# Kernel optimization log

Hardware: AMD Instinct MI355X
Metric: run time of the kernel (lower is better)

## Reference

```python
import jax, jax.numpy as jnp
import numpy as np

E, D, H, T = 8, 2048, 5632, 32768  # experts, dim, hidden_dim, total routed tokens


def setup_inputs() -> dict:
    key = jax.random.key(0)
    k_x, k1, k2, k3 = jax.random.split(key, 4)
    x = jax.random.normal(k_x, (T, D), dtype=jnp.float32)
    # trunc_normal init stds per init_weights (approx: plain normal, same scale)
    std = (2.0 / (D * 24)) ** 0.5
    w1 = jax.random.normal(k1, (E, H, D), dtype=jnp.float32) * std
    w2 = jax.random.normal(k2, (E, D, H), dtype=jnp.float32) * std
    w3 = jax.random.normal(k3, (E, H, D), dtype=jnp.float32) * std
    # tokens are pre-sorted by expert; even split 4096 tokens/expert (sums to T)
    num_tokens_per_expert = jnp.full((E,), T // E, dtype=jnp.int32)
    return {"x": x, "w1": w1, "w2": w2, "w3": w3,
            "num_tokens_per_expert": num_tokens_per_expert}


def _grouped_experts(x, w1, w2, w3, counts):
    # Faithful to _run_experts_grouped_mm: grouped GEMMs computed in bf16,
    # SwiGLU activation, cast back to x dtype.
    xb = x.astype(jnp.bfloat16)
    w1b = jnp.transpose(w1.astype(jnp.bfloat16), (0, 2, 1))  # [E, D, H]
    w3b = jnp.transpose(w3.astype(jnp.bfloat16), (0, 2, 1))  # [E, D, H]
    w2b = jnp.transpose(w2.astype(jnp.bfloat16), (0, 2, 1))  # [E, H, D]
    h1 = jax.lax.ragged_dot(xb, w1b, counts)   # [T, H]
    h3 = jax.lax.ragged_dot(xb, w3b, counts)   # [T, H]
    h = jax.nn.silu(h1) * h3                   # fused SwiGLU gate
    out = jax.lax.ragged_dot(h, w2b, counts)   # [T, D]
    return out.astype(x.dtype)


def reference(x, w1, w2, w3, num_tokens_per_expert):
    return _grouped_experts(x, w1, w2, w3, num_tokens_per_expert)
```

## Files before the change

kernel.cpp:

```cpp
#include <hip/hip_runtime.h>
#include <hip/hip_bf16.h>
#include <stdint.h>

#define TT 32768
#define DD 2048
#define HH 5632
#define NE 8

typedef __bf16 bf16;
typedef __bf16 bf16x8 __attribute__((ext_vector_type(8)));
typedef float  f32x4  __attribute__((ext_vector_type(4)));

__device__ __forceinline__ void gl16(const void* g, void* l) {
    __builtin_amdgcn_global_load_lds(
        (const __attribute__((address_space(1))) void*)g,
        (__attribute__((address_space(3))) void*)l, 16, 0, 0);
}
#define VMW(n) asm volatile("s_waitcnt vmcnt(" #n ")" ::: "memory")
#define BARRIER() __builtin_amdgcn_s_barrier()

__device__ __forceinline__ int swz(int off) { return off ^ (((off >> 7) & 3) << 4); }

__device__ __forceinline__ int expert_of(const int* counts, int row0) {
    int base = 0;
    for (int i = 0; i < NE; ++i) { int c = counts[i]; if (row0 < base + c) return i; base += c; }
    return NE - 1;
}

__global__ __launch_bounds__(256)
void k_cvt(const float* __restrict__ in, bf16* __restrict__ out, long n) {
    long i = ((long)blockIdx.x * 256 + threadIdx.x) * 8;
    const long stride = (long)gridDim.x * 256 * 8;
    for (; i < n; i += stride) {
        const float4* p = (const float4*)(in + i);
        float4 a = p[0], b = p[1];
        union { bf16 v[8]; uint4 u; } r;
        r.v[0] = (bf16)a.x; r.v[1] = (bf16)a.y; r.v[2] = (bf16)a.z; r.v[3] = (bf16)a.w;
        r.v[4] = (bf16)b.x; r.v[5] = (bf16)b.y; r.v[6] = (bf16)b.z; r.v[7] = (bf16)b.w;
        *(uint4*)(out + i) = r.u;
    }
}

__global__ __launch_bounds__(512, 2)
void k_moe1(const bf16* __restrict__ xb, const bf16* __restrict__ w1b,
            const bf16* __restrict__ w3b, const int* __restrict__ counts,
            bf16* __restrict__ h) {
    extern __shared__ __align__(16) char sm[];
    const int tid = threadIdx.x;
    const int nwg = gridDim.x;
    int wg = blockIdx.x;
    wg = (wg & 7) * (nwg >> 3) + (wg >> 3);
    const int NTN = HH / 128;
    const int mt = wg / NTN, nt = wg - mt * NTN;
    const int row0 = mt * 256, col0 = nt * 128;
    const int e = expert_of(counts, row0);

    const char *sa0, *sa1, *sa2, *sa3;
    {
        int off0 = tid * 16, off1 = 8192 + tid * 16;
        int s0 = swz(off0), s1 = swz(off1);
        sa0 = (const char*)xb + (((size_t)(row0 + (s0 >> 6)) * DD) << 1) + (s0 & 63);
        sa1 = (const char*)xb + (((size_t)(row0 + (s1 >> 6)) * DD) << 1) + (s1 & 63);
        const char* w1p = (const char*)(w1b + (size_t)e * HH * DD);
        const char* w3p = (const char*)(w3b + (size_t)e * HH * DD);
        sa2 = w1p + (((size_t)(col0 + (s0 >> 6)) * DD) << 1) + (s0 & 63);
        sa3 = w3p + (((size_t)(col0 + (s0 >> 6)) * DD) << 1) + (s0 & 63);
    }
    const int dst0 = tid * 16;

    auto stage = [&](int kt) {
        char* db = sm + ((kt & 3) << 15);
        const size_t ko = (size_t)kt << 6;
        gl16(sa0 + ko, db + dst0);
        gl16(sa1 + ko, db + 8192 + dst0);
        gl16(sa2 + ko, db + 16384 + dst0);
        gl16(sa3 + ko, db + 24576 + dst0);
    };

    const int lane = tid & 63, wv = tid >> 6;
    const int wrow = wv >> 2, wcol = wv & 3;
    const int lrow = lane & 15, kb = (lane >> 4) << 4;

    int aoff[8], boff[2];
#pragma unroll
    for (int mi = 0; mi < 8; ++mi) aoff[mi] = swz((wrow * 128 + mi * 16 + lrow) * 64 + kb);
#pragma unroll
    for (int ni = 0; ni < 2; ++ni) boff[ni] = swz((wcol * 32 + ni * 16 + lrow) * 64 + kb);

    f32x4 acc1[8][2] = {};
    f32x4 acc3[8][2] = {};

    const int NT = DD / 32;
    stage(0); stage(1); stage(2);
    for (int t = 0; t < NT; ++t) {
        BARRIER();
        if (t + 3 < NT) stage(t + 3);
        const int nf = NT - 1 - t;
        if (nf >= 3) VMW(12); else if (nf == 2) VMW(8); else if (nf == 1) VMW(4); else VMW(0);
        BARRIER();
        const char* db = sm + ((t & 3) << 15);
        bf16x8 af[8], b1[2], b3[2];
#pragma unroll
        for (int mi = 0; mi < 8; ++mi) af[mi] = *(const bf16x8*)(db + aoff[mi]);
#pragma unroll
        for (int ni = 0; ni < 2; ++ni) {
            b1[ni] = *(const bf16x8*)(db + 16384 + boff[ni]);
            b3[ni] = *(const bf16x8*)(db + 24576 + boff[ni]);
        }
        __builtin_amdgcn_s_setprio(1);
#pragma unroll
        for (int mi = 0; mi < 8; ++mi)
#pragma unroll
            for (int ni = 0; ni < 2; ++ni) {
                acc1[mi][ni] = __builtin_amdgcn_mfma_f32_16x16x32_bf16(af[mi], b1[ni], acc1[mi][ni], 0, 0, 0);
                acc3[mi][ni] = __builtin_amdgcn_mfma_f32_16x16x32_bf16(af[mi], b3[ni], acc3[mi][ni], 0, 0, 0);
            }
        __builtin_amdgcn_s_setprio(0);
    }

#pragma unroll
    for (int mi = 0; mi < 8; ++mi)
#pragma unroll
        for (int ni = 0; ni < 2; ++ni)
#pragma unroll
            for (int j = 0; j < 4; ++j) {
                int row = row0 + wrow * 128 + mi * 16 + ((lane >> 4) << 2) + j;
                int col = col0 + wcol * 32 + ni * 16 + lrow;
                float f1 = (float)(bf16)acc1[mi][ni][j];
                float f3 = (float)(bf16)acc3[mi][ni][j];
                float s = f1 / (1.0f + __expf(-f1));
                h[(size_t)row * HH + col] = (bf16)(s * f3);
            }
}

__global__ __launch_bounds__(512, 2)
void k_g2(const bf16* __restrict__ hb, const bf16* __restrict__ w2b,
          const int* __restrict__ counts, float* __restrict__ out) {
    extern __shared__ __align__(16) char sm[];
    const int tid = threadIdx.x;
    const int nwg = gridDim.x;
    int wg = blockIdx.x;
    wg = (wg & 7) * (nwg >> 3) + (wg >> 3);
    const int NTN = DD / 256;
    const int mt = wg / NTN, nt = wg - mt * NTN;
    const int row0 = mt * 256, col0 = nt * 256;
    const int e = expert_of(counts, row0);

    const char *sa0, *sa1, *sa2, *sa3;
    {
        int off0 = tid * 16, off1 = 8192 + tid * 16;
        int s0 = swz(off0), s1 = swz(off1);
        sa0 = (const char*)hb + (((size_t)(row0 + (s0 >> 6)) * HH) << 1) + (s0 & 63);
        sa1 = (const char*)hb + (((size_t)(row0 + (s1 >> 6)) * HH) << 1) + (s1 & 63);
        const char* wp = (const char*)(w2b + (size_t)e * DD * HH);
        sa2 = wp + (((size_t)(col0 + (s0 >> 6)) * HH) << 1) + (s0 & 63);
        sa3 = wp + (((size_t)(col0 + (s1 >> 6)) * HH) << 1) + (s1 & 63);
    }
    const int dst0 = tid * 16;
    auto stage = [&](int kt) {
        char* db = sm + ((kt & 3) << 15);
        const size_t ko = (size_t)kt << 6;
        gl16(sa0 + ko, db + dst0);
        gl16(sa1 + ko, db + 8192 + dst0);
        gl16(sa2 + ko, db + 16384 + dst0);
        gl16(sa3 + ko, db + 24576 + dst0);
    };

    const int lane = tid & 63, wv = tid >> 6;
    const int wrow = wv >> 2, wcol = wv & 3;
    const int lrow = lane & 15, kb = (lane >> 4) << 4;

    int aoff[8], boff[4];
#pragma unroll
    for (int mi = 0; mi < 8; ++mi) aoff[mi] = swz((wrow * 128 + mi * 16 + lrow) * 64 + kb);
#pragma unroll
    for (int ni = 0; ni < 4; ++ni) boff[ni] = swz((wcol * 64 + ni * 16 + lrow) * 64 + kb);

    f32x4 acc[8][4] = {};
    const int NT = HH / 32;
    stage(0); stage(1); stage(2);
    for (int t = 0; t < NT; ++t) {
        BARRIER();
        if (t + 3 < NT) stage(t + 3);
        const int nf = NT - 1 - t;
        if (nf >= 3) VMW(12); else if (nf == 2) VMW(8); else if (nf == 1) VMW(4); else VMW(0);
        BARRIER();
        const char* db = sm + ((t & 3) << 15);
        bf16x8 af[8], bf[4];
#pragma unroll
        for (int mi = 0; mi < 8; ++mi) af[mi] = *(const bf16x8*)(db + aoff[mi]);
#pragma unroll
        for (int ni = 0; ni < 4; ++ni) bf[ni] = *(const bf16x8*)(db + 16384 + boff[ni]);
        __builtin_amdgcn_s_setprio(1);
#pragma unroll
        for (int mi = 0; mi < 8; ++mi)
#pragma unroll
            for (int ni = 0; ni < 4; ++ni)
                acc[mi][ni] = __builtin_amdgcn_mfma_f32_16x16x32_bf16(af[mi], bf[ni], acc[mi][ni], 0, 0, 0);
        __builtin_amdgcn_s_setprio(0);
    }
#pragma unroll
    for (int mi = 0; mi < 8; ++mi)
#pragma unroll
        for (int ni = 0; ni < 4; ++ni)
#pragma unroll
            for (int j = 0; j < 4; ++j) {
                int row = row0 + wrow * 128 + mi * 16 + ((lane >> 4) << 2) + j;
                int col = col0 + wcol * 64 + ni * 16 + lrow;
                out[(size_t)row * DD + col] = (float)(bf16)acc[mi][ni][j];
            }
}

__device__ __forceinline__ void stage_b_f32(const float* __restrict__ W,
                                            int n0, int k0, int ldk,
                                            int srow, int scol,
                                            bf16* __restrict__ lB) {
#pragma unroll
    for (int r = 0; r < 4; ++r) {
        int row = r * 32 + srow;
        const float4* s = (const float4*)(W + (size_t)(n0 + row) * ldk + k0 + scol);
        float4 a = s[0], b = s[1];
        union { bf16 v[8]; uint4 u; } t;
        t.v[0] = (bf16)a.x; t.v[1] = (bf16)a.y; t.v[2] = (bf16)a.z; t.v[3] = (bf16)a.w;
        t.v[4] = (bf16)b.x; t.v[5] = (bf16)b.y; t.v[6] = (bf16)b.z; t.v[7] = (bf16)b.w;
        *(uint4*)&lB[row * 64 + scol] = t.u;
    }
}

__global__ __launch_bounds__(256, 2)
void k_gemm1_fb(const bf16* __restrict__ xb, const float* __restrict__ w1,
                const float* __restrict__ w3, const int* __restrict__ counts,
                bf16* __restrict__ hbuf) {
    __shared__ bf16 lA[128 * 64];
    __shared__ bf16 lB1[128 * 64];
    __shared__ bf16 lB3[128 * 64];
    const int tid = threadIdx.x;
    const int col0 = blockIdx.x * 128, row0 = blockIdx.y * 128;
    const int e = expert_of(counts, row0);
    const float* W1 = w1 + (size_t)e * HH * DD;
    const float* W3 = w3 + (size_t)e * HH * DD;
    const int lane = tid & 63, wv = tid >> 6;
    const int wr = wv >> 1, wc = wv & 1;
    const int lrow = lane & 15, lk8 = (lane >> 4) * 8;
    const int srow = tid >> 3, scol = (tid & 7) * 8;
    f32x4 acc1[4][4] = {}; f32x4 acc3[4][4] = {};
    for (int k0 = 0; k0 < DD; k0 += 64) {
#pragma unroll
        for (int r = 0; r < 4; ++r) {
            int row = r * 32 + srow;
            gl16(xb + (size_t)(row0 + row) * DD + k0 + scol, &lA[row * 64 + scol]);
        }
        stage_b_f32(W1, col0, k0, DD, srow, scol, lB1);
        stage_b_f32(W3, col0, k0, DD, srow, scol, lB3);
        __syncthreads();
#pragma unroll
        for (int kk = 0; kk < 64; kk += 32) {
            bf16x8 av[4], b1v[4], b3v[4];
#pragma unroll
            for (int mi = 0; mi < 4; ++mi) av[mi] = *(const bf16x8*)&lA[(wr * 64 + mi * 16 + lrow) * 64 + kk + lk8];
#pragma unroll
            for (int ni = 0; ni < 4; ++ni) {
                b1v[ni] = *(const bf16x8*)&lB1[(wc * 64 + ni * 16 + lrow) * 64 + kk + lk8];
                b3v[ni] = *(const bf16x8*)&lB3[(wc * 64 + ni * 16 + lrow) * 64 + kk + lk8];
            }
#pragma unroll
            for (int mi = 0; mi < 4; ++mi)
#pragma unroll
                for (int ni = 0; ni < 4; ++ni) {
                    acc1[mi][ni] = __builtin_amdgcn_mfma_f32_16x16x32_bf16(av[mi], b1v[ni], acc1[mi][ni], 0, 0, 0);
                    acc3[mi][ni] = __builtin_amdgcn_mfma_f32_16x16x32_bf16(av[mi], b3v[ni], acc3[mi][ni], 0, 0, 0);
                }
        }
        __syncthreads();
    }
#pragma unroll
    for (int mi = 0; mi < 4; ++mi)
#pragma unroll
        for (int ni = 0; ni < 4; ++ni)
#pragma unroll
            for (int j = 0; j < 4; ++j) {
                int row = row0 + wr * 64 + mi * 16 + ((lane >> 4) << 2) + j;
                int col = col0 + wc * 64 + ni * 16 + lrow;
                float f1 = (float)(bf16)acc1[mi][ni][j];
                float f3 = (float)(bf16)acc3[mi][ni][j];
                float sil = f1 / (1.0f + __expf(-f1));
                hbuf[(size_t)row * HH + col] = (bf16)(sil * f3);
            }
}

__global__ __launch_bounds__(256, 2)
void k_gemm2_fb(const bf16* __restrict__ hbuf, const float* __restrict__ w2,
                const int* __restrict__ counts, float* __restrict__ out) {
    __shared__ bf16 lA[128 * 64];
    __shared__ bf16 lB[128 * 64];
    const int tid = threadIdx.x;
    const int col0 = blockIdx.x * 128, row0 = blockIdx.y * 128;
    const int e = expert_of(counts, row0);
    const float* W2 = w2 + (size_t)e * DD * HH;
    const int lane = tid & 63, wv = tid >> 6;
    const int wr = wv >> 1, wc = wv & 1;
    const int lrow = lane & 15, lk8 = (lane >> 4) * 8;
    const int srow = tid >> 3, scol = (tid & 7) * 8;
    f32x4 acc[4][4] = {};
    for (int k0 = 0; k0 < HH; k0 += 64) {
#pragma unroll
        for (int r = 0; r < 4; ++r) {
            int row = r * 32 + srow;
            gl16(hbuf + (size_t)(row0 + row) * HH + k0 + scol, &lA[row * 64 + scol]);
        }
        stage_b_f32(W2, col0, k0, HH, srow, scol, lB);
        __syncthreads();
#pragma unroll
        for (int kk = 0; kk < 64; kk += 32) {
            bf16x8 av[4], bv[4];
#pragma unroll
            for (int mi = 0; mi < 4; ++mi) av[mi] = *(const bf16x8*)&lA[(wr * 64 + mi * 16 + lrow) * 64 + kk + lk8];
#pragma unroll
            for (int ni = 0; ni < 4; ++ni) bv[ni] = *(const bf16x8*)&lB[(wc * 64 + ni * 16 + lrow) * 64 + kk + lk8];
#pragma unroll
            for (int mi = 0; mi < 4; ++mi)
#pragma unroll
                for (int ni = 0; ni < 4; ++ni)
                    acc[mi][ni] = __builtin_amdgcn_mfma_f32_16x16x32_bf16(av[mi], bv[ni], acc[mi][ni], 0, 0, 0);
        }
        __syncthreads();
    }
#pragma unroll
    for (int mi = 0; mi < 4; ++mi)
#pragma unroll
        for (int ni = 0; ni < 4; ++ni)
#pragma unroll
            for (int j = 0; j < 4; ++j) {
                int row = row0 + wr * 64 + mi * 16 + ((lane >> 4) << 2) + j;
                int col = col0 + wc * 64 + ni * 16 + lrow;
                out[(size_t)row * DD + col] = (float)(bf16)acc[mi][ni][j];
            }
}

extern "C" void kernel_launch(void* const* d_in, const int* in_sizes, int n_in,
                              void* d_out, int out_size, void* d_ws, size_t ws_size,
                              hipStream_t stream) {
    const float* x      = (const float*)d_in[0];
    const float* w1     = (const float*)d_in[1];
    const float* w2     = (const float*)d_in[2];
    const float* w3     = (const float*)d_in[3];
    const int*   counts = (const int*)d_in[4];
    float* out = (float*)d_out;

    const size_t xb_b = (size_t)TT * DD * 2;
    const size_t h_b  = (size_t)TT * HH * 2;
    const size_t w_b  = (size_t)NE * HH * DD * 2;
    const size_t need_full = xb_b + h_b + 2 * w_b;

    if (ws_size >= need_full) {
        bf16* xb  = (bf16*)d_ws;
        bf16* h   = (bf16*)((char*)d_ws + xb_b);
        bf16* wsA = (bf16*)((char*)d_ws + xb_b + h_b);
        bf16* wsB = (bf16*)((char*)d_ws + xb_b + h_b + w_b);

        hipFuncSetAttribute((const void*)k_moe1, hipFuncAttributeMaxDynamicSharedMemorySize, 131072);
        hipFuncSetAttribute((const void*)k_g2,   hipFuncAttributeMaxDynamicSharedMemorySize, 131072);

        k_cvt<<<2048, 256, 0, stream>>>(x,  xb,  (long)TT * DD);
        k_cvt<<<2048, 256, 0, stream>>>(w1, wsA, (long)NE * HH * DD);
        k_cvt<<<2048, 256, 0, stream>>>(w3, wsB, (long)NE * HH * DD);
        k_moe1<<<(HH / 128) * (TT / 256), 512, 131072, stream>>>(xb, wsA, wsB, counts, h);
        k_cvt<<<2048, 256, 0, stream>>>(w2, wsA, (long)NE * DD * HH);
        k_g2<<<(DD / 256) * (TT / 256), 512, 131072, stream>>>(h, wsA, counts, out);
    } else if (ws_size >= xb_b + h_b) {
        bf16* xb   = (bf16*)d_ws;
        bf16* hbuf = (bf16*)((char*)d_ws + xb_b);
        k_cvt<<<2048, 256, 0, stream>>>(x, xb, (long)TT * DD);
        k_gemm1_fb<<<dim3(HH / 128, TT / 128), 256, 0, stream>>>(xb, w1, w3, counts, hbuf);
        k_gemm2_fb<<<dim3(DD / 128, TT / 128), 256, 0, stream>>>(hbuf, w2, counts, out);
    }
}
```

Baseline: 3.063 ms.

## Split GEMM main loops into two half-phases interleaving staging, LDS reads and MFMA

Both grouped GEMM kernels now split each K-step into two phases. Each phase loads half of the A fragments from LDS, issues half of the next global-to-LDS stage (A in the first phase, B in the second), waits on lgkmcnt behind a sched_barrier, and runs MFMAs on that half. The aim is a ping-pong style schedule that overlaps LDS reads and global loads with matrix work and lowers the number of fragment registers live at once. In exchange it adds more barriers per iteration and a more intricate vmcnt accounting at the loop tail.

```diff
diff --git a/kernel.cpp b/kernel.cpp
--- a/kernel.cpp
+++ b/kernel.cpp
@@ -17,6 +17,8 @@
         (__attribute__((address_space(3))) void*)l, 16, 0, 0);
 }
 #define VMW(n) asm volatile("s_waitcnt vmcnt(" #n ")" ::: "memory")
+#define LGKM0() do { asm volatile("s_waitcnt lgkmcnt(0)" ::: "memory"); \
+                     __builtin_amdgcn_sched_barrier(0); } while (0)
 #define BARRIER() __builtin_amdgcn_s_barrier()
 
 __device__ __forceinline__ int swz(int off) { return off ^ (((off >> 7) & 3) << 4); }
@@ -68,11 +70,15 @@
     }
     const int dst0 = tid * 16;
 
-    auto stage = [&](int kt) {
+    auto stageA = [&](int kt) {
         char* db = sm + ((kt & 3) << 15);
         const size_t ko = (size_t)kt << 6;
         gl16(sa0 + ko, db + dst0);
         gl16(sa1 + ko, db + 8192 + dst0);
+    };
+    auto stageB = [&](int kt) {
+        char* db = sm + ((kt & 3) << 15);
+        const size_t ko = (size_t)kt << 6;
         gl16(sa2 + ko, db + 16384 + dst0);
         gl16(sa3 + ko, db + 24576 + dst0);
     };
@@ -91,31 +97,55 @@
     f32x4 acc3[8][2] = {};
 
     const int NT = DD / 32;
-    stage(0); stage(1); stage(2);
+    stageA(0); stageB(0); stageA(1); stageB(1); stageA(2); stageB(2);
+    VMW(8);
+    BARRIER();
     for (int t = 0; t < NT; ++t) {
-        BARRIER();
-        if (t + 3 < NT) stage(t + 3);
-        const int nf = NT - 1 - t;
-        if (nf >= 3) VMW(12); else if (nf == 2) VMW(8); else if (nf == 1) VMW(4); else VMW(0);
-        BARRIER();
         const char* db = sm + ((t & 3) << 15);
-        bf16x8 af[8], b1[2], b3[2];
-#pragma unroll
-        for (int mi = 0; mi < 8; ++mi) af[mi] = *(const bf16x8*)(db + aoff[mi]);
-#pragma unroll
-        for (int ni = 0; ni < 2; ++ni) {
-            b1[ni] = *(const bf16x8*)(db + 16384 + boff[ni]);
-            b3[ni] = *(const bf16x8*)(db + 24576 + boff[ni]);
-        }
-        __builtin_amdgcn_s_setprio(1);
-#pragma unroll
-        for (int mi = 0; mi < 8; ++mi)
+        bf16x8 b1[2], b3[2];
+        {
+            bf16x8 af[4];
+#pragma unroll
+            for (int mi = 0; mi < 4; ++mi) af[mi] = *(const bf16x8*)(db + aoff[mi]);
 #pragma unroll
             for (int ni = 0; ni < 2; ++ni) {
-                acc1[mi][ni] = __builtin_amdgcn_mfma_f32_16x16x32_bf16(af[mi], b1[ni], acc1[mi][ni], 0, 0, 0);
-                acc3[mi][ni] = __builtin_amdgcn_mfma_f32_16x16x32_bf16(af[mi], b3[ni], acc3[mi][ni], 0, 0, 0);
-            }
-        __builtin_amdgcn_s_setprio(0);
+                b1[ni] = *(const bf16x8*)(db + 16384 + boff[ni]);
+                b3[ni] = *(const bf16x8*)(db + 24576 + boff[ni]);
+            }
+            if (t + 3 < NT) stageA(t + 3);
+            BARRIER();
+            LGKM0();
+            __builtin_amdgcn_s_setprio(1);
+#pragma unroll
+            for (int mi = 0; mi < 4; ++mi)
+#pragma unroll
+                for (int ni = 0; ni < 2; ++ni) {
+                    acc1[mi][ni] = __builtin_amdgcn_mfma_f32_16x16x32_bf16(af[mi], b1[ni], acc1[mi][ni], 0, 0, 0);
+                    acc3[mi][ni] = __builtin_amdgcn_mfma_f32_16x16x32_bf16(af[mi], b3[ni], acc3[mi][ni], 0, 0, 0);
+                }
+            __builtin_amdgcn_s_setprio(0);
+            BARRIER();
+        }
+        {
+            bf16x8 af[4];
+#pragma unroll
+            for (int mi = 0; mi < 4; ++mi) af[mi] = *(const bf16x8*)(db + aoff[mi + 4]);
+            if (t + 3 < NT) { stageB(t + 3); VMW(8); }
+            else if (t == NT - 3) { VMW(4); }
+            else if (t == NT - 2) { VMW(0); }
+            BARRIER();
+            LGKM0();
+            __builtin_amdgcn_s_setprio(1);
+#pragma unroll
+            for (int mi = 0; mi < 4; ++mi)
+#pragma unroll
+                for (int ni = 0; ni < 2; ++ni) {
+                    acc1[mi + 4][ni] = __builtin_amdgcn_mfma_f32_16x16x32_bf16(af[mi], b1[ni], acc1[mi + 4][ni], 0, 0, 0);
+                    acc3[mi + 4][ni] = __builtin_amdgcn_mfma_f32_16x16x32_bf16(af[mi], b3[ni], acc3[mi + 4][ni], 0, 0, 0);
+                }
+            __builtin_amdgcn_s_setprio(0);
+            BARRIER();
+        }
     }
 
 #pragma unroll
@@ -157,11 +187,15 @@
         sa3 = wp + (((size_t)(col0 + (s1 >> 6)) * HH) << 1) + (s1 & 63);
     }
     const int dst0 = tid * 16;
-    auto stage = [&](int kt) {
+    auto stageA = [&](int kt) {
         char* db = sm + ((kt & 3) << 15);
         const size_t ko = (size_t)kt << 6;
         gl16(sa0 + ko, db + dst0);
         gl16(sa1 + ko, db + 8192 + dst0);
+    };
+    auto stageB = [&](int kt) {
+        char* db = sm + ((kt & 3) << 15);
+        const size_t ko = (size_t)kt << 6;
         gl16(sa2 + ko, db + 16384 + dst0);
         gl16(sa3 + ko, db + 24576 + dst0);
     };
@@ -178,26 +212,48 @@
 
     f32x4 acc[8][4] = {};
     const int NT = HH / 32;
-    stage(0); stage(1); stage(2);
+    stageA(0); stageB(0); stageA(1); stageB(1); stageA(2); stageB(2);
+    VMW(8);
+    BARRIER();
     for (int t = 0; t < NT; ++t) {
-        BARRIER();
-        if (t + 3 < NT) stage(t + 3);
-        const int nf = NT - 1 - t;
-        if (nf >= 3) VMW(12); else if (nf == 2) VMW(8); else if (nf == 1) VMW(4); else VMW(0);
-        BARRIER();
         const char* db = sm + ((t & 3) << 15);
-        bf16x8 af[8], bf[4];
-#pragma unroll
-        for (int mi = 0; mi < 8; ++mi) af[mi] = *(const bf16x8*)(db + aoff[mi]);
-#pragma unroll
-        for (int ni = 0; ni < 4; ++ni) bf[ni] = *(const bf16x8*)(db + 16384 + boff[ni]);
-        __builtin_amdgcn_s_setprio(1);
-#pragma unroll
-        for (int mi = 0; mi < 8; ++mi)
-#pragma unroll
-            for (int ni = 0; ni < 4; ++ni)
-                acc[mi][ni] = __builtin_amdgcn_mfma_f32_16x16x32_bf16(af[mi], bf[ni], acc[mi][ni], 0, 0, 0);
-        __builtin_amdgcn_s_setprio(0);
+        bf16x8 bf[4];
+        {
+            bf16x8 af[4];
+#pragma unroll
+            for (int mi = 0; mi < 4; ++mi) af[mi] = *(const bf16x8*)(db + aoff[mi]);
+#pragma unroll
+            for (int ni = 0; ni < 4; ++ni) bf[ni] = *(const bf16x8*)(db + 16384 + boff[ni]);
+            if (t + 3 < NT) stageA(t + 3);
+            BARRIER();
+            LGKM0();
+            __builtin_amdgcn_s_setprio(1);
+#pragma unroll
+            for (int mi = 0; mi < 4; ++mi)
+#pragma unroll
+                for (int ni = 0; ni < 4; ++ni)
+                    acc[mi][ni] = __builtin_amdgcn_mfma_f32_16x16x32_bf16(af[mi], bf[ni], acc[mi][ni], 0, 0, 0);
+            __builtin_amdgcn_s_setprio(0);
+            BARRIER();
+        }
+        {
+            bf16x8 af[4];
+#pragma unroll
+            for (int mi = 0; mi < 4; ++mi) af[mi] = *(const bf16x8*)(db + aoff[mi + 4]);
+            if (t + 3 < NT) { stageB(t + 3); VMW(8); }
+            else if (t == NT - 3) { VMW(4); }
+            else if (t == NT - 2) { VMW(0); }
+            BARRIER();
+            LGKM0();
+            __builtin_amdgcn_s_setprio(1);
+#pragma unroll
+            for (int mi = 0; mi < 4; ++mi)
+#pragma unroll
+                for (int ni = 0; ni < 4; ++ni)
+                    acc[mi + 4][ni] = __builtin_amdgcn_mfma_f32_16x16x32_bf16(af[mi], bf[ni], acc[mi + 4][ni], 0, 0, 0);
+            __builtin_amdgcn_s_setprio(0);
+            BARRIER();
+        }
     }
 #pragma unroll
     for (int mi = 0; mi < 8; ++mi)
```

Measured after the change: 2.904 ms. 5.2% less time.
